# Kernel tuning notes

Hardware: AMD Instinct MI355X
Metric: run time of the kernel (lower is better)

Reference implementation:

```python
import jax, jax.numpy as jnp
import numpy as np

D = 2048
B = 32768
EPS = 1e-5


def _branch_params(key, d):
    k1, k2 = jax.random.split(key)
    s1 = 1.0 / np.sqrt(d)
    return dict(
        W1=jax.random.uniform(k1, (d, d), jnp.float32, -s1, s1),
        b1=jnp.zeros((d,), jnp.float32),
        ln_g=jnp.ones((d,), jnp.float32),
        ln_b=jnp.zeros((d,), jnp.float32),
        W2=jax.random.uniform(k2, (2, d), jnp.float32, -s1, s1),
        b2=jnp.zeros((2,), jnp.float32),
    )


def setup_inputs() -> dict:
    key = jax.random.key(0)
    kx, kf, ka, kr = jax.random.split(key, 4)
    x = jax.random.normal(kx, (B, D), jnp.float32)
    inp = {"x": x}
    for name, k in (("first", kf), ("fake", ka), ("real", kr)):
        p = _branch_params(k, D)
        for pn, pv in p.items():
            inp[f"{name}_{pn}"] = pv
    return inp


def _branch(x, W1, b1, g, be, W2, b2):
    # Linear(d,d) -> LayerNorm(d) -> ReLU -> Linear(d,2); Dropout is identity at eval.
    h = x @ W1.T + b1                                   # [B, D]
    mu = jnp.mean(h, axis=-1, keepdims=True)
    var = jnp.mean(jnp.square(h - mu), axis=-1, keepdims=True)
    h = (h - mu) * jax.lax.rsqrt(var + EPS) * g + be
    h = jax.nn.relu(h)
    return h @ W2.T + b2                                # [B, 2]


def reference(x,
              first_W1, first_b1, first_ln_g, first_ln_b, first_W2, first_b2,
              fake_W1, fake_b1, fake_ln_g, fake_ln_b, fake_W2, fake_b2,
              real_W1, real_b1, real_ln_g, real_ln_b, real_W2, real_b2):
    first_logits = _branch(x, first_W1, first_b1, first_ln_g, first_ln_b, first_W2, first_b2)
    route = jnp.argmax(first_logits, axis=1)            # [B], 0 -> fake expert, else real
    fake_logits = _branch(x, fake_W1, fake_b1, fake_ln_g, fake_ln_b, fake_W2, fake_b2)
    real_logits = _branch(x, real_W1, real_b1, real_ln_g, real_ln_b, real_W2, real_b2)
    final_logits = jnp.where((route == 0)[:, None], fake_logits, real_logits)  # [B, 2]
    return final_logits
```

## Files before the change

kernel.cpp:

```cpp
#include <hip/hip_runtime.h>

#define BD 32768
#define DD 2048
#define LN_EPS 1e-5f
#define MARGIN 0.03f
#define UCAP 8192
#define IDX_CAP 33280

typedef unsigned short u16;
typedef unsigned int u32;
typedef __bf16 bf16x8 __attribute__((ext_vector_type(8)));
typedef float floatx4 __attribute__((ext_vector_type(4)));

__device__ inline u16 f2bf(float f) {
    u32 u = __builtin_bit_cast(u32, f);
    u32 r = (u + 0x7fffu + ((u >> 16) & 1u)) >> 16;
    return (u16)r;
}
__device__ inline float bf2f(u16 h) {
    return __builtin_bit_cast(float, ((u32)h) << 16);
}
__device__ inline void bf2x2(u32 p, float& lo, float& hi) {
    lo = __builtin_bit_cast(float, p << 16);
    hi = __builtin_bit_cast(float, p & 0xffff0000u);
}

__device__ inline void lds16(const void* g, void* l) {
    __builtin_amdgcn_global_load_lds(
        (const __attribute__((address_space(1))) u32*)g,
        (__attribute__((address_space(3))) u32*)l, 16, 0, 0);
}

__global__ __launch_bounds__(256) void zero_misc(int* idx_all, int* u_idx, int* ctrl) {
    int t = blockIdx.x * 256 + threadIdx.x;
    if (t < IDX_CAP) idx_all[t] = 0;
    if (t < UCAP) u_idx[t] = 0;
    if (t < 8) ctrl[t] = 0;
}

__global__ __launch_bounds__(256) void split_f32(const float* __restrict__ in,
                                                 u16* __restrict__ hi,
                                                 u16* __restrict__ lo, int n4) {
    int i = blockIdx.x * 256 + threadIdx.x;
    if (i >= n4) return;
    float4 f = ((const float4*)in)[i];
    u16 h0 = f2bf(f.x), h1 = f2bf(f.y), h2 = f2bf(f.z), h3 = f2bf(f.w);
    u16 l0 = f2bf(f.x - bf2f(h0)), l1 = f2bf(f.y - bf2f(h1));
    u16 l2 = f2bf(f.z - bf2f(h2)), l3 = f2bf(f.w - bf2f(h3));
    ((ushort4*)hi)[i] = make_ushort4(h0, h1, h2, h3);
    ((ushort4*)lo)[i] = make_ushort4(l0, l1, l2, l3);
}

__global__ __launch_bounds__(256) void split_w3(const float* __restrict__ w0,
                                                const float* __restrict__ w1,
                                                const float* __restrict__ w2,
                                                u16* h0, u16* l0p,
                                                u16* h1, u16* l1p,
                                                u16* h2, u16* l2p) {
    int i = blockIdx.x * 256 + threadIdx.x;
    int m = blockIdx.y;
    const float* in = (m == 0) ? w0 : (m == 1) ? w1 : w2;
    u16* hi = (m == 0) ? h0 : (m == 1) ? h1 : h2;
    u16* lo = (m == 0) ? l0p : (m == 1) ? l1p : l2p;
    float4 f = ((const float4*)in)[i];
    u16 a0 = f2bf(f.x), a1 = f2bf(f.y), a2 = f2bf(f.z), a3 = f2bf(f.w);
    u16 b0 = f2bf(f.x - bf2f(a0)), b1 = f2bf(f.y - bf2f(a1));
    u16 b2 = f2bf(f.z - bf2f(a2)), b3 = f2bf(f.w - bf2f(a3));
    ((ushort4*)hi)[i] = make_ushort4(a0, a1, a2, a3);
    ((ushort4*)lo)[i] = make_ushort4(b0, b1, b2, b3);
}

template <int IDX, int DUAL>
__global__ __launch_bounds__(512, 2) void gemm256(const u16* __restrict__ A,
                                                  const u16* __restrict__ B1,
                                                  const u16* __restrict__ B2,
                                                  u16* __restrict__ C,
                                                  const int* __restrict__ ridx,
                                                  const int* __restrict__ ctrl) {
    const int nwg = (int)(gridDim.x * gridDim.y);
    const int wg0 = (int)(blockIdx.y * gridDim.x + blockIdx.x);
    const int chunk = nwg >> 3;
    const int swz = (wg0 & 7) * chunk + (wg0 >> 3);
    const size_t bm = (size_t)(swz >> 3) * 256;
    const size_t bn = (size_t)(swz & 7) * 256;

    const u16* Bp = B1;
    if (DUAL) {
        int nf_pad = ctrl[3];
        int limit = nf_pad + (BD - ctrl[2]);
        if ((int)bm >= limit) return;
        if ((int)bm >= nf_pad) Bp = B2;
    }

    __shared__ alignas(16) u16 smem[65536];
    const int tid = threadIdx.x;
    const int lane = tid & 63;
    const int wave = tid >> 6;
    const int wr = wave >> 2, wc = wave & 3;
    const int m16 = lane & 15, q4 = lane >> 4;

    const int srow = tid >> 3;
    const int kq = ((tid & 7) ^ (srow & 7)) * 8;
    const int tid8 = tid * 8;
    size_t aOff[4], bOff[4];
#pragma unroll
    for (int s = 0; s < 4; ++s) {
        int row = s * 64 + srow;
        int g = IDX ? ridx[bm + row] : (int)(bm + row);
        aOff[s] = (size_t)g * DD + kq;
        bOff[s] = (size_t)(bn + row) * DD + kq;
    }

    const int slot0 = ((q4) ^ (m16 & 7)) * 8;
    const int slot1 = ((4 + q4) ^ (m16 & 7)) * 8;
    const int aFr = (wr * 128 + m16) * 64;
    const int bFr = 16384 + (wc * 64 + m16) * 64;

    floatx4 acc[8][4] = {};

    lds16(Bp + bOff[0], &smem[16384 + 0 * 4096 + tid8]);
    lds16(Bp + bOff[1], &smem[16384 + 1 * 4096 + tid8]);
    lds16(A + aOff[0], &smem[0 * 4096 + tid8]);
    lds16(A + aOff[2], &smem[2 * 4096 + tid8]);
    lds16(Bp + bOff[2], &smem[16384 + 2 * 4096 + tid8]);
    lds16(Bp + bOff[3], &smem[16384 + 3 * 4096 + tid8]);
    lds16(A + aOff[1], &smem[1 * 4096 + tid8]);
    lds16(A + aOff[3], &smem[3 * 4096 + tid8]);

    int base = 0;
    const int NT = DD / 64;
    for (int t = 0; t < NT; ++t) {
        const int nbase = base ^ 32768;
        const int k0n = (t + 1) * 64;
        const bool pre = (t + 1 < NT);

        bf16x8 bfr[2][4];
#pragma unroll
        for (int p = 0; p < 4; ++p) {
            if (pre) {
                if (p == 0) {
                    lds16(Bp + bOff[0] + k0n, &smem[nbase + 16384 + 0 * 4096 + tid8]);
                    lds16(Bp + bOff[1] + k0n, &smem[nbase + 16384 + 1 * 4096 + tid8]);
                } else if (p == 1) {
                    lds16(A + aOff[0] + k0n, &smem[nbase + 0 * 4096 + tid8]);
                    lds16(A + aOff[2] + k0n, &smem[nbase + 2 * 4096 + tid8]);
                } else if (p == 2) {
                    lds16(Bp + bOff[2] + k0n, &smem[nbase + 16384 + 2 * 4096 + tid8]);
                    lds16(Bp + bOff[3] + k0n, &smem[nbase + 16384 + 3 * 4096 + tid8]);
                } else {
                    lds16(A + aOff[1] + k0n, &smem[nbase + 1 * 4096 + tid8]);
                    lds16(A + aOff[3] + k0n, &smem[nbase + 3 * 4096 + tid8]);
                }
            }
            if (p == 0) {
                if (pre) asm volatile("s_waitcnt vmcnt(4)" ::: "memory");
                else     asm volatile("s_waitcnt vmcnt(2)" ::: "memory");
            } else if (p == 2) {
                if (pre) asm volatile("s_waitcnt vmcnt(6)" ::: "memory");
                else     asm volatile("s_waitcnt vmcnt(0)" ::: "memory");
            }
            __builtin_amdgcn_s_barrier();
            __builtin_amdgcn_sched_barrier(0);

            if (p == 0) {
#pragma unroll
                for (int j = 0; j < 4; ++j) {
                    bfr[0][j] = *(const bf16x8*)&smem[base + bFr + j * 1024 + slot0];
                    bfr[1][j] = *(const bf16x8*)&smem[base + bFr + j * 1024 + slot1];
                }
            }
            bf16x8 a0k0 = *(const bf16x8*)&smem[base + aFr + (2 * p) * 1024 + slot0];
            bf16x8 a0k1 = *(const bf16x8*)&smem[base + aFr + (2 * p) * 1024 + slot1];
            bf16x8 a1k0 = *(const bf16x8*)&smem[base + aFr + (2 * p + 1) * 1024 + slot0];
            bf16x8 a1k1 = *(const bf16x8*)&smem[base + aFr + (2 * p + 1) * 1024 + slot1];
            asm volatile("s_waitcnt lgkmcnt(0)" ::: "memory");
            __builtin_amdgcn_sched_barrier(0);

            __builtin_amdgcn_s_setprio(1);
#pragma unroll
            for (int j = 0; j < 4; ++j) {
                acc[2 * p][j]     = __builtin_amdgcn_mfma_f32_16x16x32_bf16(a0k0, bfr[0][j], acc[2 * p][j], 0, 0, 0);
                acc[2 * p][j]     = __builtin_amdgcn_mfma_f32_16x16x32_bf16(a0k1, bfr[1][j], acc[2 * p][j], 0, 0, 0);
                acc[2 * p + 1][j] = __builtin_amdgcn_mfma_f32_16x16x32_bf16(a1k0, bfr[0][j], acc[2 * p + 1][j], 0, 0, 0);
                acc[2 * p + 1][j] = __builtin_amdgcn_mfma_f32_16x16x32_bf16(a1k1, bfr[1][j], acc[2 * p + 1][j], 0, 0, 0);
            }
            __builtin_amdgcn_s_setprio(0);
            __builtin_amdgcn_s_barrier();
        }
        base = nbase;
    }

#pragma unroll
    for (int i = 0; i < 8; ++i) {
#pragma unroll
        for (int r = 0; r < 4; ++r) {
            size_t grow = bm + wr * 128 + i * 16 + q4 * 4 + r;
            u16* crow = C + grow * DD + bn + wc * 64 + m16;
#pragma unroll
            for (int j = 0; j < 4; ++j) crow[j * 16] = f2bf(acc[i][j][r]);
        }
    }
}

__global__ __launch_bounds__(256) void gemm_split(const u16* __restrict__ Ahi,
                                                  const u16* __restrict__ Alo,
                                                  const u16* __restrict__ Bhi,
                                                  const u16* __restrict__ Blo,
                                                  float* __restrict__ C,
                                                  const int* __restrict__ ridx,
                                                  const int* __restrict__ ctrl) {
    const int tid = threadIdx.x;
    const size_t bm = (size_t)blockIdx.y * 128;
    const size_t bn = (size_t)blockIdx.x * 128;

    int u = ctrl[1]; if (u > UCAP) u = UCAP;
    if ((int)bm >= u) return;

    __shared__ alignas(16) u16 smem[4 * 4096];
    const int lane = tid & 63;
    const int wave = tid >> 6;
    const int wm = (wave >> 1) * 64, wn = (wave & 1) * 64;
    const int m16 = lane & 15, q = lane >> 4;
    const int swz = (q ^ ((m16 >> 1) & 3)) * 8;

    int aRow[2], kqv[2];
    size_t bOff[2];
#pragma unroll
    for (int s = 0; s < 2; ++s) {
        int e = s * 256 + tid;
        int row = e >> 2;
        int c = e & 3;
        kqv[s] = (c ^ ((row >> 1) & 3)) * 8;
        aRow[s] = ridx[bm + row];
        bOff[s] = (size_t)(bn + row) * DD;
    }

    floatx4 acc[4][4] = {};

    for (int k0 = 0; k0 < DD; k0 += 32) {
#pragma unroll
        for (int s = 0; s < 2; ++s) {
            int e = s * 256 + tid;
            size_t aoff = (size_t)aRow[s] * DD + k0 + kqv[s];
            size_t boff = bOff[s] + k0 + kqv[s];
            lds16(Ahi + aoff, &smem[e * 8]);
            lds16(Bhi + boff, &smem[4096 + e * 8]);
            lds16(Alo + aoff, &smem[8192 + e * 8]);
            lds16(Blo + boff, &smem[12288 + e * 8]);
        }
        __syncthreads();

        bf16x8 ah[4], bh[4], al[4], bl[4];
#pragma unroll
        for (int i = 0; i < 4; ++i) {
            ah[i] = *(const bf16x8*)&smem[(wm + i * 16 + m16) * 32 + swz];
            bh[i] = *(const bf16x8*)&smem[4096 + (wn + i * 16 + m16) * 32 + swz];
            al[i] = *(const bf16x8*)&smem[8192 + (wm + i * 16 + m16) * 32 + swz];
            bl[i] = *(const bf16x8*)&smem[12288 + (wn + i * 16 + m16) * 32 + swz];
        }
#pragma unroll
        for (int i = 0; i < 4; ++i)
#pragma unroll
            for (int j = 0; j < 4; ++j) {
                acc[i][j] = __builtin_amdgcn_mfma_f32_16x16x32_bf16(ah[i], bh[j], acc[i][j], 0, 0, 0);
                acc[i][j] = __builtin_amdgcn_mfma_f32_16x16x32_bf16(ah[i], bl[j], acc[i][j], 0, 0, 0);
                acc[i][j] = __builtin_amdgcn_mfma_f32_16x16x32_bf16(al[i], bh[j], acc[i][j], 0, 0, 0);
            }
        __syncthreads();
    }

#pragma unroll
    for (int i = 0; i < 4; ++i)
#pragma unroll
        for (int r = 0; r < 4; ++r) {
            size_t grow = bm + wm + i * 16 + q * 4 + r;
            float* crow = C + grow * DD + bn + wn + m16;
#pragma unroll
            for (int j = 0; j < 4; ++j) crow[j * 16] = acc[i][j][r];
        }
}

__device__ inline void stage_params(float* __restrict__ sp,
                                    const float* __restrict__ b1,
                                    const float* __restrict__ g,
                                    const float* __restrict__ be,
                                    const float* __restrict__ W2, int tid) {
#pragma unroll
    for (int k = 0; k < 2; ++k) {
        int idx = (k * 256 + tid) * 4;
        *(float4*)&sp[idx]          = *(const float4*)&b1[idx];
        *(float4*)&sp[2048 + idx]   = *(const float4*)&g[idx];
        *(float4*)&sp[4096 + idx]   = *(const float4*)&be[idx];
        *(float4*)&sp[6144 + idx]   = *(const float4*)&W2[idx];
        *(float4*)&sp[8192 + idx]   = *(const float4*)&W2[2048 + idx];
    }
}

__device__ inline void ln_row(const u16* __restrict__ hr,
                              const float* __restrict__ sp,
                              int lane, float b20, float b21,
                              float& L0, float& L1) {
    const int cb = lane * 8;
    uint4 h0 = *(const uint4*)(hr + 0 * 512 + cb);
    uint4 h1 = *(const uint4*)(hr + 1 * 512 + cb);
    uint4 h2 = *(const uint4*)(hr + 2 * 512 + cb);
    uint4 h3 = *(const uint4*)(hr + 3 * 512 + cb);

    float sum = 0.f, sumsq = 0.f;
#define LN_STATS(HV, C)                                                        \
    {                                                                          \
        int col = (C) * 512 + cb;                                              \
        float4 b0 = *(const float4*)(sp + col);                                \
        float4 b4 = *(const float4*)(sp + col + 4);                            \
        float f0, f1, f2, f3, f4, f5, f6, f7;                                  \
        bf2x2(HV.x, f0, f1); bf2x2(HV.y, f2, f3);                              \
        bf2x2(HV.z, f4, f5); bf2x2(HV.w, f6, f7);                              \
        f0 += b0.x; f1 += b0.y; f2 += b0.z; f3 += b0.w;                        \
        f4 += b4.x; f5 += b4.y; f6 += b4.z; f7 += b4.w;                        \
        sum += ((f0 + f1) + (f2 + f3)) + ((f4 + f5) + (f6 + f7));              \
        sumsq += ((f0 * f0 + f1 * f1) + (f2 * f2 + f3 * f3)) +                 \
                 ((f4 * f4 + f5 * f5) + (f6 * f6 + f7 * f7));                  \
    }
    LN_STATS(h0, 0) LN_STATS(h1, 1) LN_STATS(h2, 2) LN_STATS(h3, 3)
#undef LN_STATS
#pragma unroll
    for (int off = 32; off > 0; off >>= 1) {
        sum += __shfl_xor(sum, off);
        sumsq += __shfl_xor(sumsq, off);
    }
    const float mu = sum * (1.f / 2048.f);
    const float var = sumsq * (1.f / 2048.f) - mu * mu;
    const float rstd = rsqrtf(var + LN_EPS);

    float l0 = 0.f, l1 = 0.f;
#define LN_HEAD(HV, C)                                                         \
    {                                                                          \
        int col = (C) * 512 + cb;                                              \
        float4 b0 = *(const float4*)(sp + col);                                \
        float4 b4 = *(const float4*)(sp + col + 4);                            \
        float4 g0 = *(const float4*)(sp + 2048 + col);                         \
        float4 g4 = *(const float4*)(sp + 2048 + col + 4);                     \
        float4 e0 = *(const float4*)(sp + 4096 + col);                         \
        float4 e4 = *(const float4*)(sp + 4096 + col + 4);                     \
        float4 w00 = *(const float4*)(sp + 6144 + col);                        \
        float4 w04 = *(const float4*)(sp + 6144 + col + 4);                    \
        float4 w10 = *(const float4*)(sp + 8192 + col);                        \
        float4 w14 = *(const float4*)(sp + 8192 + col + 4);                    \
        float f0, f1, f2, f3, f4, f5, f6, f7, hn;                              \
        bf2x2(HV.x, f0, f1); bf2x2(HV.y, f2, f3);                              \
        bf2x2(HV.z, f4, f5); bf2x2(HV.w, f6, f7);                              \
        hn = fmaxf(((f0 + b0.x) - mu) * rstd * g0.x + e0.x, 0.f); l0 += hn * w00.x; l1 += hn * w10.x; \
        hn = fmaxf(((f1 + b0.y) - mu) * rstd * g0.y + e0.y, 0.f); l0 += hn * w00.y; l1 += hn * w10.y; \
        hn = fmaxf(((f2 + b0.z) - mu) * rstd * g0.z + e0.z, 0.f); l0 += hn * w00.z; l1 += hn * w10.z; \
        hn = fmaxf(((f3 + b0.w) - mu) * rstd * g0.w + e0.w, 0.f); l0 += hn * w00.w; l1 += hn * w10.w; \
        hn = fmaxf(((f4 + b4.x) - mu) * rstd * g4.x + e4.x, 0.f); l0 += hn * w04.x; l1 += hn * w14.x; \
        hn = fmaxf(((f5 + b4.y) - mu) * rstd * g4.y + e4.y, 0.f); l0 += hn * w04.y; l1 += hn * w14.y; \
        hn = fmaxf(((f6 + b4.z) - mu) * rstd * g4.z + e4.z, 0.f); l0 += hn * w04.z; l1 += hn * w14.z; \
        hn = fmaxf(((f7 + b4.w) - mu) * rstd * g4.w + e4.w, 0.f); l0 += hn * w04.w; l1 += hn * w14.w; \
    }
    LN_HEAD(h0, 0) LN_HEAD(h1, 1) LN_HEAD(h2, 2) LN_HEAD(h3, 3)
#undef LN_HEAD
#pragma unroll
    for (int off = 32; off > 0; off >>= 1) {
        l0 += __shfl_xor(l0, off);
        l1 += __shfl_xor(l1, off);
    }
    L0 = l0 + b20;
    L1 = l1 + b21;
}

__device__ inline void ln_core(const float* __restrict__ hr,
                               const float* __restrict__ b1,
                               const float* __restrict__ g,
                               const float* __restrict__ be,
                               const float* __restrict__ W2,
                               const float* __restrict__ b2,
                               int lane, float& L0, float& L1) {
    float v[32];
    float sum = 0.f, sumsq = 0.f;
#pragma unroll
    for (int i = 0; i < 8; ++i) {
        int col = i * 256 + lane * 4;
        float4 t = *(const float4*)(hr + col);
        float4 bb = *(const float4*)(b1 + col);
        t.x += bb.x; t.y += bb.y; t.z += bb.z; t.w += bb.w;
        v[i * 4 + 0] = t.x; v[i * 4 + 1] = t.y; v[i * 4 + 2] = t.z; v[i * 4 + 3] = t.w;
        sum += t.x + t.y + t.z + t.w;
        sumsq += t.x * t.x + t.y * t.y + t.z * t.z + t.w * t.w;
    }
#pragma unroll
    for (int off = 32; off > 0; off >>= 1) {
        sum += __shfl_xor(sum, off);
        sumsq += __shfl_xor(sumsq, off);
    }
    const float mu = sum * (1.f / 2048.f);
    const float var = sumsq * (1.f / 2048.f) - mu * mu;
    const float rstd = rsqrtf(var + LN_EPS);

    float l0 = 0.f, l1 = 0.f;
#pragma unroll
    for (int i = 0; i < 8; ++i) {
        int col = i * 256 + lane * 4;
        float4 gg = *(const float4*)(g + col);
        float4 bbe = *(const float4*)(be + col);
        float4 w0 = *(const float4*)(W2 + col);
        float4 w1 = *(const float4*)(W2 + DD + col);
        float hn;
        hn = fmaxf((v[i * 4 + 0] - mu) * rstd * gg.x + bbe.x, 0.f); l0 += hn * w0.x; l1 += hn * w1.x;
        hn = fmaxf((v[i * 4 + 1] - mu) * rstd * gg.y + bbe.y, 0.f); l0 += hn * w0.y; l1 += hn * w1.y;
        hn = fmaxf((v[i * 4 + 2] - mu) * rstd * gg.z + bbe.z, 0.f); l0 += hn * w0.z; l1 += hn * w1.z;
        hn = fmaxf((v[i * 4 + 3] - mu) * rstd * gg.w + bbe.w, 0.f); l0 += hn * w0.w; l1 += hn * w1.w;
    }
#pragma unroll
    for (int off = 32; off > 0; off >>= 1) {
        l0 += __shfl_xor(l0, off);
        l1 += __shfl_xor(l1, off);
    }
    L0 = l0 + b2[0];
    L1 = l1 + b2[1];
}

__global__ __launch_bounds__(256) void ln_route(const u16* __restrict__ h,
                                                const float* __restrict__ b1,
                                                const float* __restrict__ g,
                                                const float* __restrict__ be,
                                                const float* __restrict__ W2,
                                                const float* __restrict__ b2,
                                                int* __restrict__ route,
                                                int* __restrict__ ctrl,
                                                int* __restrict__ u_idx) {
    __shared__ float sp[5 * 2048];
    __shared__ int blk_nf;
    const int tid = threadIdx.x;
    if (tid == 0) blk_nf = 0;
    stage_params(sp, b1, g, be, W2, tid);
    __syncthreads();
    const int wave = tid >> 6, lane = tid & 63;
    const int r = blockIdx.x * 4 + wave;
    float l0, l1;
    ln_row(h + (size_t)r * DD, sp, lane, b2[0], b2[1], l0, l1);
    if (lane == 0) {
        int rt = (l0 >= l1) ? 0 : 1;
        route[r] = rt;
        if (rt == 0) atomicAdd(&blk_nf, 1);
        if (fabsf(l0 - l1) < MARGIN) {
            int p = atomicAdd(&ctrl[1], 1);
            if (p < UCAP) u_idx[p] = r;
        }
    }
    __syncthreads();
    if (tid == 0 && blk_nf) atomicAdd(&ctrl[0], blk_nf);
}

__global__ __launch_bounds__(256) void ln_fixup(const float* __restrict__ h,
                                                const float* __restrict__ b1,
                                                const float* __restrict__ g,
                                                const float* __restrict__ be,
                                                const float* __restrict__ W2,
                                                const float* __restrict__ b2,
                                                int* __restrict__ route,
                                                int* __restrict__ ctrl,
                                                const int* __restrict__ u_idx) {
    const int wave = threadIdx.x >> 6, lane = threadIdx.x & 63;
    const int r = blockIdx.x * 4 + wave;
    int u = ctrl[1]; if (u > UCAP) u = UCAP;
    if (r >= u) return;
    const int orig = u_idx[r];
    float l0, l1;
    ln_core(h + (size_t)r * DD, b1, g, be, W2, b2, lane, l0, l1);
    if (lane == 0) {
        int rt = (l0 >= l1) ? 0 : 1;
        int old = route[orig];
        if (rt != old) {
            atomicAdd(&ctrl[0], rt == 0 ? 1 : -1);
            route[orig] = rt;
        }
    }
}

__global__ void init_ctrl(int* ctrl) {
    int nf = ctrl[0];
    ctrl[2] = nf;
    ctrl[3] = (nf + 255) & ~255;
    ctrl[4] = 0;
    ctrl[5] = ctrl[3];
}

__global__ __launch_bounds__(256) void compact(const int* __restrict__ route,
                                               int* __restrict__ ctrl,
                                               int* __restrict__ idx_all) {
    const int row = blockIdx.x * 256 + threadIdx.x;
    const int lane = threadIdx.x & 63;
    const bool isf = (route[row] == 0);
    unsigned long long m = __ballot(isf);
    int nfw = __popcll(m);
    int baseF = 0, baseR = 0;
    if (lane == 0) {
        baseF = atomicAdd(&ctrl[4], nfw);
        baseR = atomicAdd(&ctrl[5], 64 - nfw);
    }
    baseF = __shfl(baseF, 0);
    baseR = __shfl(baseR, 0);
    unsigned long long lt = (lane == 0) ? 0ull : ((~0ull) >> (64 - lane));
    int pre = __popcll(m & lt);
    int pos = isf ? (baseF + pre) : (baseR + (lane - pre));
    idx_all[pos] = row;
}

__global__ __launch_bounds__(256) void ln_final(const u16* __restrict__ h,
                                                const float* __restrict__ b1f, const float* __restrict__ gf,
                                                const float* __restrict__ bef, const float* __restrict__ W2f,
                                                const float* __restrict__ b2f,
                                                const float* __restrict__ b1r, const float* __restrict__ gr,
                                                const float* __restrict__ ber, const float* __restrict__ W2r,
                                                const float* __restrict__ b2r,
                                                const int* __restrict__ ctrl,
                                                const int* __restrict__ idx_all,
                                                float* __restrict__ out) {
    const int nf = ctrl[2], nf_pad = ctrl[3];
    const int limit = nf_pad + (BD - nf);
    const int base = blockIdx.x * 4;
    bool fake;
    if (base < nf) fake = true;
    else if (base >= nf_pad && base < limit) fake = false;
    else return;

    __shared__ float sp[5 * 2048];
    const int tid = threadIdx.x;
    stage_params(sp, fake ? b1f : b1r, fake ? gf : gr, fake ? bef : ber,
                 fake ? W2f : W2r, tid);
    __syncthreads();
    const int wave = tid >> 6, lane = tid & 63;
    const int r = base + wave;
    if (fake ? (r < nf) : (r < limit)) {
        const float* b2 = fake ? b2f : b2r;
        float l0, l1;
        ln_row(h + (size_t)r * DD, sp, lane, b2[0], b2[1], l0, l1);
        if (lane == 0) {
            int orig = idx_all[r];
            out[(size_t)orig * 2 + 0] = l0;
            out[(size_t)orig * 2 + 1] = l1;
        }
    }
}

extern "C" void kernel_launch(void* const* d_in, const int* in_sizes, int n_in,
                              void* d_out, int out_size, void* d_ws, size_t ws_size,
                              hipStream_t stream) {
    const float* x = (const float*)d_in[0];
    const float* W1[3] = {(const float*)d_in[1], (const float*)d_in[7], (const float*)d_in[13]};
    const float* b1[3] = {(const float*)d_in[2], (const float*)d_in[8], (const float*)d_in[14]};
    const float* lg[3] = {(const float*)d_in[3], (const float*)d_in[9], (const float*)d_in[15]};
    const float* lb[3] = {(const float*)d_in[4], (const float*)d_in[10], (const float*)d_in[16]};
    const float* W2[3] = {(const float*)d_in[5], (const float*)d_in[11], (const float*)d_in[17]};
    const float* b2[3] = {(const float*)d_in[6], (const float*)d_in[12], (const float*)d_in[18]};

    char* ws = (char*)d_ws;
    size_t off = 0;
    u16* x_hi = (u16*)(ws + off); off += (size_t)BD * DD * 2;
    u16* x_lo = (u16*)(ws + off); off += (size_t)BD * DD * 2;
    u16* w_hi[3];
    u16* w_lo[3];
    for (int i = 0; i < 3; ++i) { w_hi[i] = (u16*)(ws + off); off += (size_t)DD * DD * 2; }
    for (int i = 0; i < 3; ++i) { w_lo[i] = (u16*)(ws + off); off += (size_t)DD * DD * 2; }
    u16* h16 = (u16*)(ws + off); off += (size_t)IDX_CAP * DD * 2;
    float* hfix = (float*)(ws + off); off += (size_t)UCAP * DD * 4;
    int* route = (int*)(ws + off); off += (size_t)BD * 4;
    int* idx_all = (int*)(ws + off); off += (size_t)IDX_CAP * 4;
    int* u_idx = (int*)(ws + off); off += (size_t)UCAP * 4;
    int* ctrl = (int*)(ws + off); off += 64;

    zero_misc<<<(IDX_CAP + 255) / 256, 256, 0, stream>>>(idx_all, u_idx, ctrl);

    split_f32<<<(BD * DD / 4) / 256, 256, 0, stream>>>(x, x_hi, x_lo, BD * DD / 4);
    split_w3<<<dim3((DD * DD / 4) / 256, 3), 256, 0, stream>>>(
        W1[0], W1[1], W1[2], w_hi[0], w_lo[0], w_hi[1], w_lo[1], w_hi[2], w_lo[2]);

    gemm256<0, 0><<<dim3(DD / 256, BD / 256), 512, 0, stream>>>(
        x_hi, w_hi[0], nullptr, h16, nullptr, nullptr);
    ln_route<<<BD / 4, 256, 0, stream>>>(h16, b1[0], lg[0], lb[0], W2[0], b2[0],
                                         route, ctrl, u_idx);

    gemm_split<<<dim3(DD / 128, UCAP / 128), 256, 0, stream>>>(
        x_hi, x_lo, w_hi[0], w_lo[0], hfix, u_idx, ctrl);
    ln_fixup<<<UCAP / 4, 256, 0, stream>>>(hfix, b1[0], lg[0], lb[0], W2[0], b2[0],
                                           route, ctrl, u_idx);

    init_ctrl<<<1, 1, 0, stream>>>(ctrl);
    compact<<<BD / 256, 256, 0, stream>>>(route, ctrl, idx_all);

    gemm256<1, 1><<<dim3(DD / 256, BD / 256 + 1), 512, 0, stream>>>(
        x_hi, w_hi[1], w_hi[2], h16, idx_all, ctrl);

    ln_final<<<IDX_CAP / 4, 256, 0, stream>>>(
        h16, b1[1], lg[1], lb[1], W2[1], b2[1],
        b1[2], lg[2], lb[2], W2[2], b2[2],
        ctrl, idx_all, (float*)d_out);
}
```

Baseline: 1.187 ms.

## Compute x low-part only for uncertain rows and double-buffer both GEMM pipelines

The low bf16 residual of x is now computed only for the uncertain rows selected by the router, gathered into a compact buffer, instead of for the whole input. This removes a full-size write of the low half. gemm256 now issues each whole next tile in one batch with a single wait and barrier pair per K step, instead of spreading the prefetch across four phases with a barrier in each. gemm_split gains double-buffered LDS with prefetch, replacing its synchronous load-then-sync loop. The trade-offs are one extra kernel launch, double the LDS in gemm_split, and coarser overlap of loads with MFMA work in gemm256.

```diff
diff --git a/kernel.cpp b/kernel.cpp
--- a/kernel.cpp
+++ b/kernel.cpp
@@ -38,17 +38,32 @@
     if (t < 8) ctrl[t] = 0;
 }
 
-__global__ __launch_bounds__(256) void split_f32(const float* __restrict__ in,
-                                                 u16* __restrict__ hi,
-                                                 u16* __restrict__ lo, int n4) {
+__global__ __launch_bounds__(256) void split_xhi(const float* __restrict__ in,
+                                                 u16* __restrict__ hi, int n4) {
     int i = blockIdx.x * 256 + threadIdx.x;
     if (i >= n4) return;
     float4 f = ((const float4*)in)[i];
-    u16 h0 = f2bf(f.x), h1 = f2bf(f.y), h2 = f2bf(f.z), h3 = f2bf(f.w);
-    u16 l0 = f2bf(f.x - bf2f(h0)), l1 = f2bf(f.y - bf2f(h1));
-    u16 l2 = f2bf(f.z - bf2f(h2)), l3 = f2bf(f.w - bf2f(h3));
-    ((ushort4*)hi)[i] = make_ushort4(h0, h1, h2, h3);
-    ((ushort4*)lo)[i] = make_ushort4(l0, l1, l2, l3);
+    ((ushort4*)hi)[i] = make_ushort4(f2bf(f.x), f2bf(f.y), f2bf(f.z), f2bf(f.w));
+}
+
+__global__ __launch_bounds__(256) void split_xlo(const float* __restrict__ x,
+                                                 const int* __restrict__ u_idx,
+                                                 const int* __restrict__ ctrl,
+                                                 u16* __restrict__ xlo) {
+    int u = ctrl[1]; if (u > UCAP) u = UCAP;
+    int r = blockIdx.x;
+    if (r >= u) return;
+    int orig = u_idx[r];
+    const float4* src = (const float4*)(x + (size_t)orig * DD);
+    ushort4* dst = (ushort4*)(xlo + (size_t)r * DD);
+    int i = threadIdx.x;
+#pragma unroll
+    for (int k = 0; k < 2; ++k, i += 256) {
+        float4 f = src[i];
+        u16 h0 = f2bf(f.x), h1 = f2bf(f.y), h2 = f2bf(f.z), h3 = f2bf(f.w);
+        dst[i] = make_ushort4(f2bf(f.x - bf2f(h0)), f2bf(f.y - bf2f(h1)),
+                              f2bf(f.z - bf2f(h2)), f2bf(f.w - bf2f(h3)));
+    }
 }
 
 __global__ __launch_bounds__(256) void split_w3(const float* __restrict__ w0,
@@ -118,64 +133,44 @@
 
     floatx4 acc[8][4] = {};
 
-    lds16(Bp + bOff[0], &smem[16384 + 0 * 4096 + tid8]);
-    lds16(Bp + bOff[1], &smem[16384 + 1 * 4096 + tid8]);
-    lds16(A + aOff[0], &smem[0 * 4096 + tid8]);
-    lds16(A + aOff[2], &smem[2 * 4096 + tid8]);
-    lds16(Bp + bOff[2], &smem[16384 + 2 * 4096 + tid8]);
-    lds16(Bp + bOff[3], &smem[16384 + 3 * 4096 + tid8]);
-    lds16(A + aOff[1], &smem[1 * 4096 + tid8]);
-    lds16(A + aOff[3], &smem[3 * 4096 + tid8]);
+#define STAGE_TILE(DB, K0)                                              \
+    lds16(A + aOff[0] + (K0), &smem[(DB) + 0 * 4096 + tid8]);           \
+    lds16(A + aOff[1] + (K0), &smem[(DB) + 1 * 4096 + tid8]);           \
+    lds16(A + aOff[2] + (K0), &smem[(DB) + 2 * 4096 + tid8]);           \
+    lds16(A + aOff[3] + (K0), &smem[(DB) + 3 * 4096 + tid8]);           \
+    lds16(Bp + bOff[0] + (K0), &smem[(DB) + 16384 + 0 * 4096 + tid8]);  \
+    lds16(Bp + bOff[1] + (K0), &smem[(DB) + 16384 + 1 * 4096 + tid8]);  \
+    lds16(Bp + bOff[2] + (K0), &smem[(DB) + 16384 + 2 * 4096 + tid8]);  \
+    lds16(Bp + bOff[3] + (K0), &smem[(DB) + 16384 + 3 * 4096 + tid8]);
+
+    STAGE_TILE(0, 0)
 
     int base = 0;
     const int NT = DD / 64;
     for (int t = 0; t < NT; ++t) {
         const int nbase = base ^ 32768;
-        const int k0n = (t + 1) * 64;
-        const bool pre = (t + 1 < NT);
+        __builtin_amdgcn_s_barrier();
+        if (t + 1 < NT) {
+            STAGE_TILE(nbase, (t + 1) * 64)
+            asm volatile("s_waitcnt vmcnt(8)" ::: "memory");
+        } else {
+            asm volatile("s_waitcnt vmcnt(0)" ::: "memory");
+        }
+        __builtin_amdgcn_s_barrier();
+        __builtin_amdgcn_sched_barrier(0);
 
         bf16x8 bfr[2][4];
 #pragma unroll
+        for (int j = 0; j < 4; ++j) {
+            bfr[0][j] = *(const bf16x8*)&smem[base + bFr + j * 1024 + slot0];
+            bfr[1][j] = *(const bf16x8*)&smem[base + bFr + j * 1024 + slot1];
+        }
+#pragma unroll
         for (int p = 0; p < 4; ++p) {
-            if (pre) {
-                if (p == 0) {
-                    lds16(Bp + bOff[0] + k0n, &smem[nbase + 16384 + 0 * 4096 + tid8]);
-                    lds16(Bp + bOff[1] + k0n, &smem[nbase + 16384 + 1 * 4096 + tid8]);
-                } else if (p == 1) {
-                    lds16(A + aOff[0] + k0n, &smem[nbase + 0 * 4096 + tid8]);
-                    lds16(A + aOff[2] + k0n, &smem[nbase + 2 * 4096 + tid8]);
-                } else if (p == 2) {
-                    lds16(Bp + bOff[2] + k0n, &smem[nbase + 16384 + 2 * 4096 + tid8]);
-                    lds16(Bp + bOff[3] + k0n, &smem[nbase + 16384 + 3 * 4096 + tid8]);
-                } else {
-                    lds16(A + aOff[1] + k0n, &smem[nbase + 1 * 4096 + tid8]);
-                    lds16(A + aOff[3] + k0n, &smem[nbase + 3 * 4096 + tid8]);
-                }
-            }
-            if (p == 0) {
-                if (pre) asm volatile("s_waitcnt vmcnt(4)" ::: "memory");
-                else     asm volatile("s_waitcnt vmcnt(2)" ::: "memory");
-            } else if (p == 2) {
-                if (pre) asm volatile("s_waitcnt vmcnt(6)" ::: "memory");
-                else     asm volatile("s_waitcnt vmcnt(0)" ::: "memory");
-            }
-            __builtin_amdgcn_s_barrier();
-            __builtin_amdgcn_sched_barrier(0);
-
-            if (p == 0) {
-#pragma unroll
-                for (int j = 0; j < 4; ++j) {
-                    bfr[0][j] = *(const bf16x8*)&smem[base + bFr + j * 1024 + slot0];
-                    bfr[1][j] = *(const bf16x8*)&smem[base + bFr + j * 1024 + slot1];
-                }
-            }
             bf16x8 a0k0 = *(const bf16x8*)&smem[base + aFr + (2 * p) * 1024 + slot0];
             bf16x8 a0k1 = *(const bf16x8*)&smem[base + aFr + (2 * p) * 1024 + slot1];
             bf16x8 a1k0 = *(const bf16x8*)&smem[base + aFr + (2 * p + 1) * 1024 + slot0];
             bf16x8 a1k1 = *(const bf16x8*)&smem[base + aFr + (2 * p + 1) * 1024 + slot1];
-            asm volatile("s_waitcnt lgkmcnt(0)" ::: "memory");
-            __builtin_amdgcn_sched_barrier(0);
-
             __builtin_amdgcn_s_setprio(1);
 #pragma unroll
             for (int j = 0; j < 4; ++j) {
@@ -185,10 +180,10 @@
                 acc[2 * p + 1][j] = __builtin_amdgcn_mfma_f32_16x16x32_bf16(a1k1, bfr[1][j], acc[2 * p + 1][j], 0, 0, 0);
             }
             __builtin_amdgcn_s_setprio(0);
-            __builtin_amdgcn_s_barrier();
         }
         base = nbase;
     }
+#undef STAGE_TILE
 
 #pragma unroll
     for (int i = 0; i < 8; ++i) {
@@ -216,14 +211,14 @@
     int u = ctrl[1]; if (u > UCAP) u = UCAP;
     if ((int)bm >= u) return;
 
-    __shared__ alignas(16) u16 smem[4 * 4096];
+    __shared__ alignas(16) u16 smem[2 * 16384];
     const int lane = tid & 63;
     const int wave = tid >> 6;
     const int wm = (wave >> 1) * 64, wn = (wave & 1) * 64;
     const int m16 = lane & 15, q = lane >> 4;
-    const int swz = (q ^ ((m16 >> 1) & 3)) * 8;
-
-    int aRow[2], kqv[2];
+    const int swzf = (q ^ ((m16 >> 1) & 3)) * 8;
+
+    int aRow[2], gRow[2], kqv[2];
     size_t bOff[2];
 #pragma unroll
     for (int s = 0; s < 2; ++s) {
@@ -232,32 +227,46 @@
         int c = e & 3;
         kqv[s] = (c ^ ((row >> 1) & 3)) * 8;
         aRow[s] = ridx[bm + row];
+        gRow[s] = (int)bm + row;
         bOff[s] = (size_t)(bn + row) * DD;
     }
 
     floatx4 acc[4][4] = {};
 
-    for (int k0 = 0; k0 < DD; k0 += 32) {
-#pragma unroll
-        for (int s = 0; s < 2; ++s) {
-            int e = s * 256 + tid;
-            size_t aoff = (size_t)aRow[s] * DD + k0 + kqv[s];
-            size_t boff = bOff[s] + k0 + kqv[s];
-            lds16(Ahi + aoff, &smem[e * 8]);
-            lds16(Bhi + boff, &smem[4096 + e * 8]);
-            lds16(Alo + aoff, &smem[8192 + e * 8]);
-            lds16(Blo + boff, &smem[12288 + e * 8]);
-        }
-        __syncthreads();
+#define SPLIT_STAGE(DB, K0)                                                       \
+    lds16(Ahi + (size_t)aRow[0] * DD + (K0) + kqv[0], &smem[(DB) + tid * 8]);     \
+    lds16(Ahi + (size_t)aRow[1] * DD + (K0) + kqv[1], &smem[(DB) + 2048 + tid * 8]); \
+    lds16(Bhi + bOff[0] + (K0) + kqv[0], &smem[(DB) + 4096 + tid * 8]);           \
+    lds16(Bhi + bOff[1] + (K0) + kqv[1], &smem[(DB) + 6144 + tid * 8]);           \
+    lds16(Alo + (size_t)gRow[0] * DD + (K0) + kqv[0], &smem[(DB) + 8192 + tid * 8]); \
+    lds16(Alo + (size_t)gRow[1] * DD + (K0) + kqv[1], &smem[(DB) + 10240 + tid * 8]); \
+    lds16(Blo + bOff[0] + (K0) + kqv[0], &smem[(DB) + 12288 + tid * 8]);          \
+    lds16(Blo + bOff[1] + (K0) + kqv[1], &smem[(DB) + 14336 + tid * 8]);
+
+    SPLIT_STAGE(0, 0)
+    int base = 0;
+    const int NTS = DD / 32;
+    for (int t = 0; t < NTS; ++t) {
+        const int nbase = base ^ 16384;
+        __builtin_amdgcn_s_barrier();
+        if (t + 1 < NTS) {
+            SPLIT_STAGE(nbase, (t + 1) * 32)
+            asm volatile("s_waitcnt vmcnt(8)" ::: "memory");
+        } else {
+            asm volatile("s_waitcnt vmcnt(0)" ::: "memory");
+        }
+        __builtin_amdgcn_s_barrier();
+        __builtin_amdgcn_sched_barrier(0);
 
         bf16x8 ah[4], bh[4], al[4], bl[4];
 #pragma unroll
         for (int i = 0; i < 4; ++i) {
-            ah[i] = *(const bf16x8*)&smem[(wm + i * 16 + m16) * 32 + swz];
-            bh[i] = *(const bf16x8*)&smem[4096 + (wn + i * 16 + m16) * 32 + swz];
-            al[i] = *(const bf16x8*)&smem[8192 + (wm + i * 16 + m16) * 32 + swz];
-            bl[i] = *(const bf16x8*)&smem[12288 + (wn + i * 16 + m16) * 32 + swz];
-        }
+            ah[i] = *(const bf16x8*)&smem[base + (wm + i * 16 + m16) * 32 + swzf];
+            bh[i] = *(const bf16x8*)&smem[base + 4096 + (wn + i * 16 + m16) * 32 + swzf];
+            al[i] = *(const bf16x8*)&smem[base + 8192 + (wm + i * 16 + m16) * 32 + swzf];
+            bl[i] = *(const bf16x8*)&smem[base + 12288 + (wn + i * 16 + m16) * 32 + swzf];
+        }
+        __builtin_amdgcn_s_setprio(1);
 #pragma unroll
         for (int i = 0; i < 4; ++i)
 #pragma unroll
@@ -266,8 +275,10 @@
                 acc[i][j] = __builtin_amdgcn_mfma_f32_16x16x32_bf16(ah[i], bl[j], acc[i][j], 0, 0, 0);
                 acc[i][j] = __builtin_amdgcn_mfma_f32_16x16x32_bf16(al[i], bh[j], acc[i][j], 0, 0, 0);
             }
-        __syncthreads();
-    }
+        __builtin_amdgcn_s_setprio(0);
+        base = nbase;
+    }
+#undef SPLIT_STAGE
 
 #pragma unroll
     for (int i = 0; i < 4; ++i)
@@ -558,7 +569,7 @@
     char* ws = (char*)d_ws;
     size_t off = 0;
     u16* x_hi = (u16*)(ws + off); off += (size_t)BD * DD * 2;
-    u16* x_lo = (u16*)(ws + off); off += (size_t)BD * DD * 2;
+    u16* x_lo = (u16*)(ws + off); off += (size_t)UCAP * DD * 2;
     u16* w_hi[3];
     u16* w_lo[3];
     for (int i = 0; i < 3; ++i) { w_hi[i] = (u16*)(ws + off); off += (size_t)DD * DD * 2; }
@@ -572,7 +583,7 @@
 
     zero_misc<<<(IDX_CAP + 255) / 256, 256, 0, stream>>>(idx_all, u_idx, ctrl);
 
-    split_f32<<<(BD * DD / 4) / 256, 256, 0, stream>>>(x, x_hi, x_lo, BD * DD / 4);
+    split_xhi<<<(BD * DD / 4) / 256, 256, 0, stream>>>(x, x_hi, BD * DD / 4);
     split_w3<<<dim3((DD * DD / 4) / 256, 3), 256, 0, stream>>>(
         W1[0], W1[1], W1[2], w_hi[0], w_lo[0], w_hi[1], w_lo[1], w_hi[2], w_lo[2]);
 
@@ -581,6 +592,7 @@
     ln_route<<<BD / 4, 256, 0, stream>>>(h16, b1[0], lg[0], lb[0], W2[0], b2[0],
                                          route, ctrl, u_idx);
 
+    split_xlo<<<UCAP, 256, 0, stream>>>(x, u_idx, ctrl, x_lo);
     gemm_split<<<dim3(DD / 128, UCAP / 128), 256, 0, stream>>>(
         x_hi, x_lo, w_hi[0], w_lo[0], hfix, u_idx, ctrl);
     ln_fixup<<<UCAP / 4, 256, 0, stream>>>(hfix, b1[0], lg[0], lb[0], W2[0], b2[0],
```

Result: slower. 1.240 ms (+4.4%).
